# Optimization experiments

Hardware: AMD Instinct MI355X
Metric: run time of the kernel (lower is better)

Reference implementation:

```python
import jax, jax.numpy as jnp
import numpy as np

HIDDEN = 2048
NUM_HEADS = 16
HEAD_DIM = HIDDEN // NUM_HEADS


def setup_inputs() -> dict:
    key = jax.random.key(0)
    ks = jax.random.split(key, 10)
    B, S = 2, 2048
    scale = 1.0 / np.sqrt(HIDDEN)
    inp = {
        "x": jax.random.normal(ks[0], (B, S, HIDDEN), dtype=jnp.float32),
        "attention_mask": jnp.zeros((B, S), dtype=jnp.float32),
        "Wq": jax.random.normal(ks[1], (HIDDEN, HIDDEN), dtype=jnp.float32) * scale,
        "bq": jnp.zeros((HIDDEN,), dtype=jnp.float32),
        "Wk": jax.random.normal(ks[2], (HIDDEN, HIDDEN), dtype=jnp.float32) * scale,
        "bk": jnp.zeros((HIDDEN,), dtype=jnp.float32),
        "Wv": jax.random.normal(ks[3], (HIDDEN, HIDDEN), dtype=jnp.float32) * scale,
        "bv": jnp.zeros((HIDDEN,), dtype=jnp.float32),
        "Wo": jax.random.normal(ks[4], (HIDDEN, HIDDEN), dtype=jnp.float32) * scale,
        "bo": jnp.zeros((HIDDEN,), dtype=jnp.float32),
    }
    return inp


def _split_heads(t):
    # [B, S, H*D] -> [B, H, S, D]
    B, S, _ = t.shape
    return t.reshape(B, S, NUM_HEADS, HEAD_DIM).transpose(0, 2, 1, 3)


def reference(x, attention_mask, Wq, bq, Wk, bk, Wv, bv, Wo, bo):
    B, S, _ = x.shape
    # Linear layers: y = x @ W^T + b (torch nn.Linear convention)
    q = _split_heads(x @ Wq.T + bq)  # [B, H, S, D]
    k = _split_heads(x @ Wk.T + bk)
    v = _split_heads(x @ Wv.T + bv)
    scale = 1.0 / jnp.sqrt(jnp.asarray(HEAD_DIM, dtype=x.dtype))
    scores = jnp.einsum("bhqd,bhkd->bhqk", q, k) * scale  # [B, H, S, S]
    scores = scores + attention_mask[:, None, None, :]  # additive mask broadcast
    attn = jax.nn.softmax(scores, axis=-1)
    out = jnp.einsum("bhqk,bhkd->bhqd", attn, v)  # [B, H, S, D]
    out = out.transpose(0, 2, 1, 3).reshape(B, S, HIDDEN)
    return out @ Wo.T + bo
```

## Files before the change

kernel.cpp:

```cpp
#include <hip/hip_runtime.h>
#include <math.h>

constexpr int S_LEN = 2048;
constexpr int HID   = 2048;
constexpr int NH    = 16;
constexpr int HD    = 128;

typedef __attribute__((ext_vector_type(8))) short short8;
typedef __attribute__((ext_vector_type(4))) float floatx4;

static __device__ __forceinline__ ushort f2bf(float f) {
  union { float f; unsigned u; } v; v.f = f;
  unsigned r = (v.u + 0x7fffu + ((v.u >> 16) & 1u)) >> 16;
  return (ushort)r;
}
static __device__ __forceinline__ ushort f2bf_fast(float f) {
  union { float f; unsigned u; } v; v.f = f;
  return (ushort)((v.u + 0x8000u) >> 16);
}

static __device__ __forceinline__ void glds16(const ushort* g, ushort* l) {
  __builtin_amdgcn_global_load_lds(
      (const __attribute__((address_space(1))) void*)g,
      (__attribute__((address_space(3))) void*)l, 16, 0, 0);
}

static __device__ __forceinline__ void barrier_raw() {
  __builtin_amdgcn_s_barrier();
  asm volatile("" ::: "memory");
}

static __device__ __forceinline__ void cvt4(ushort* dst, const float* src, size_t i) {
  const float4 v = ((const float4*)src)[i];
  ushort4 u = {f2bf(v.x), f2bf(v.y), f2bf(v.z), f2bf(v.w)};
  ((ushort4*)dst)[i] = u;
}

__global__ __launch_bounds__(256)
void convert_all(const float* __restrict__ x,
                 const float* __restrict__ wq, const float* __restrict__ wk,
                 const float* __restrict__ wv, const float* __restrict__ wo,
                 ushort* __restrict__ xb, ushort* __restrict__ wqb,
                 ushort* __restrict__ wkb, ushort* __restrict__ wvb,
                 ushort* __restrict__ wob) {
  const size_t gid = blockIdx.x * 256 + threadIdx.x;
  const size_t T = gridDim.x * 256;
  const size_t NX = (size_t)4096 * HID / 4;
  const size_t NW = (size_t)HID * HID / 4;
  for (size_t i = gid; i < NX; i += T) cvt4(xb, x, i);
  for (size_t i = gid; i < NW; i += T) {
    cvt4(wqb, wq, i);
    cvt4(wkb, wk, i);
    cvt4(wvb, wv, i);
    cvt4(wob, wo, i);
  }
}

template <int MODE>
__device__ __forceinline__
void gemm8_core(ushort* __restrict__ lds,
                const ushort* __restrict__ A, const ushort* __restrict__ W,
                const float* __restrict__ bias, void* __restrict__ Cv,
                int m0, int n0) {
  constexpr int NT = HID / 64;

  const int tid  = threadIdx.x;
  const int lane = tid & 63;
  const int w    = tid >> 6;
  const int wm   = w >> 1, wn = w & 1;
  const int n16  = lane & 15, q4 = lane >> 4;
  const int n7   = n16 & 7;

  const int srow  = lane >> 3;
  const int sslot = lane & 7;
  const int sl    = sslot ^ srow;

  const ushort* asrc[4];
  const ushort* bsrc[2];
  #pragma unroll
  for (int c = 0; c < 4; ++c)
    asrc[c] = A + (size_t)(m0 + c*64 + w*8 + srow) * HID + sl*8;
  #pragma unroll
  for (int c = 0; c < 2; ++c)
    bsrc[c] = W + (size_t)(n0 + c*64 + w*8 + srow) * HID + sl*8;

  const int wofs = w * 512;

  floatx4 acc[4][4];
  #pragma unroll
  for (int i = 0; i < 4; ++i)
    #pragma unroll
    for (int j = 0; j < 4; ++j) acc[i][j] = (floatx4)0.f;

  auto stage_tile = [&](int t, ushort* base) {
    #pragma unroll
    for (int c = 0; c < 4; ++c)
      glds16(asrc[c] + (size_t)t*64, base + c*4096 + wofs);
    #pragma unroll
    for (int c = 0; c < 2; ++c)
      glds16(bsrc[c] + (size_t)t*64, base + 16384 + c*4096 + wofs);
  };

  stage_tile(0, lds);
  stage_tile(1, lds + 24576);

  for (int t = 0; t < NT; ++t) {
    if (t == NT - 1) asm volatile("s_waitcnt vmcnt(0)" ::: "memory");
    else             asm volatile("s_waitcnt vmcnt(6)" ::: "memory");
    barrier_raw();

    if (t + 2 < NT) stage_tile(t + 2, lds + (size_t)((t + 2) % 3) * 24576);

    const ushort* cA = lds + (size_t)(t % 3) * 24576;
    const ushort* cB = cA + 16384;

    short8 af[2][4], bf[2][4];
    #pragma unroll
    for (int kc = 0; kc < 2; ++kc) {
      #pragma unroll
      for (int mt = 0; mt < 4; ++mt)
        af[kc][mt] = *(const short8*)(cA + (wm*64 + mt*16 + n16)*64
                                         + (((kc*4 + q4) ^ n7) * 8));
      #pragma unroll
      for (int nt = 0; nt < 4; ++nt)
        bf[kc][nt] = *(const short8*)(cB + (wn*64 + nt*16 + n16)*64
                                         + (((kc*4 + q4) ^ n7) * 8));
    }
    #pragma unroll
    for (int kc = 0; kc < 2; ++kc) {
      __builtin_amdgcn_s_setprio(1);
      #pragma unroll
      for (int mt = 0; mt < 4; ++mt)
        #pragma unroll
        for (int nt = 0; nt < 4; ++nt)
          acc[mt][nt] = __builtin_amdgcn_mfma_f32_16x16x32_bf16(
              af[kc][mt], bf[kc][nt], acc[mt][nt], 0, 0, 0);
      __builtin_amdgcn_s_setprio(0);
    }
  }

  float bv4[4];
  #pragma unroll
  for (int nt = 0; nt < 4; ++nt) bv4[nt] = bias[n0 + wn*64 + nt*16 + n16];

  if constexpr (MODE == 2) {
    barrier_raw();
    ushort* dumpT = lds;
    constexpr int SP = 264;
    #pragma unroll
    for (int mt = 0; mt < 4; ++mt)
      #pragma unroll
      for (int nt = 0; nt < 4; ++nt) {
        uint2 pk;
        pk.x = (uint)f2bf(acc[mt][nt][0] + bv4[nt]) |
               ((uint)f2bf(acc[mt][nt][1] + bv4[nt]) << 16);
        pk.y = (uint)f2bf(acc[mt][nt][2] + bv4[nt]) |
               ((uint)f2bf(acc[mt][nt][3] + bv4[nt]) << 16);
        const int dl  = wn*64 + nt*16 + n16;
        const int sl0 = wm*64 + mt*16 + q4*4;
        *(uint2*)&dumpT[dl*SP + sl0] = pk;
      }
    barrier_raw();
    const int dl = (w & 1)*64 + lane;
    const int s0 = (w >> 1)*64;
    ushort* dp = (ushort*)Cv +
        ((size_t)((m0 >> 11)*NH + (n0 >> 7))*HD + dl)*S_LEN + (m0 & 2047) + s0;
    #pragma unroll
    for (int j = 0; j < 8; ++j)
      *(uint4*)&dp[j*8] = *(const uint4*)&dumpT[dl*SP + s0 + j*8];
  } else {
    #pragma unroll
    for (int mt = 0; mt < 4; ++mt)
      #pragma unroll
      for (int nt = 0; nt < 4; ++nt)
        #pragma unroll
        for (int r = 0; r < 4; ++r) {
          const int row = m0 + wm*64 + mt*16 + q4*4 + r;
          const int col = n0 + wn*64 + nt*16 + n16;
          if (MODE == 1)
            ((ushort*)Cv)[(size_t)row * HID + col] = f2bf(acc[mt][nt][r] + bv4[nt]);
          else
            ((float*)Cv)[(size_t)row * HID + col] = acc[mt][nt][r] + bv4[nt];
        }
  }
}

static __device__ __forceinline__ void tile_coords(int& m0, int& n0) {
  const int id = blockIdx.y * gridDim.x + blockIdx.x;
  const int s  = ((id & 7) << 5) | (id >> 3);
  m0 = (s >> 4) * 256;
  n0 = (s & 15) * 128;
}

__global__ __launch_bounds__(512, 2)
void gemm_qkv(const ushort* __restrict__ xb,
              const ushort* __restrict__ wqb, const ushort* __restrict__ wkb,
              const ushort* __restrict__ wvb,
              const float* __restrict__ bq, const float* __restrict__ bk,
              const float* __restrict__ bv,
              ushort* __restrict__ qb, ushort* __restrict__ kb_,
              ushort* __restrict__ vt) {
  __shared__ __align__(16) ushort lds[73728];
  int m0, n0; tile_coords(m0, n0);
  if (blockIdx.z == 0)      gemm8_core<1>(lds, xb, wqb, bq, qb,  m0, n0);
  else if (blockIdx.z == 1) gemm8_core<1>(lds, xb, wkb, bk, kb_, m0, n0);
  else                      gemm8_core<2>(lds, xb, wvb, bv, vt,  m0, n0);
}

__global__ __launch_bounds__(512, 2)
void gemm_o(const ushort* __restrict__ ao, const ushort* __restrict__ wob,
            const float* __restrict__ bo, float* __restrict__ out) {
  __shared__ __align__(16) ushort lds[73728];
  int m0, n0; tile_coords(m0, n0);
  gemm8_core<0>(lds, ao, wob, bo, out, m0, n0);
}

__global__ __launch_bounds__(256, 2)
void attn_mfma(const ushort* __restrict__ qb, const ushort* __restrict__ kbuf,
               const ushort* __restrict__ vtb, const float* __restrict__ mask,
               ushort* __restrict__ ao) {
  __shared__ __align__(16) ushort SM[25600];

  const int tid  = threadIdx.x;
  const int w    = tid >> 6;
  const int lane = tid & 63;
  const int n16  = lane & 15;
  const int q4   = lane >> 4;
  const int n7   = n16 & 7;
  const int b  = blockIdx.y >> 4;
  const int h  = blockIdx.y & 15;
  const int q0 = blockIdx.x * 128;
  const float scale = 0.08838834764831845f;

  ushort* Ks = SM;
  ushort* Vs = SM + 8192;
  ushort* Pw = SM + 16384 + w * 2304;

  short8 aq[2][4];
  #pragma unroll
  for (int mt = 0; mt < 2; ++mt) {
    const ushort* qrow = qb + (size_t)(b*S_LEN + q0 + w*32 + mt*16 + n16)*HID + h*HD;
    #pragma unroll
    for (int kc = 0; kc < 4; ++kc)
      aq[mt][kc] = *(const short8*)(qrow + kc*32 + q4*8);
  }

  const ushort* ksrc[4];
  const ushort* vsrc[4];
  #pragma unroll
  for (int i = 0; i < 4; ++i) {
    const int p = (w*4 + i)*64 + lane;
    { const int rho = p >> 4, pc = p & 15;
      const int cl = (pc & 8) | ((pc ^ rho) & 7);
      ksrc[i] = kbuf + (size_t)(b*S_LEN + rho)*HID + h*HD + cl*8; }
    { const int rho = p >> 3, pc = p & 7;
      const int cl = (pc ^ rho) & 7;
      vsrc[i] = vtb + ((size_t)(b*NH + h)*HD + rho)*S_LEN + cl*8; }
  }

  floatx4 oacc[2][8];
  float lp[2][4];
  #pragma unroll
  for (int mt = 0; mt < 2; ++mt) {
    #pragma unroll
    for (int dt = 0; dt < 8; ++dt) oacc[mt][dt] = (floatx4)0.f;
    #pragma unroll
    for (int r = 0; r < 4; ++r) lp[mt][r] = 0.f;
  }

  #pragma unroll
  for (int i = 0; i < 4; ++i) glds16(ksrc[i], Ks + (w*4 + i)*512);
  #pragma unroll
  for (int i = 0; i < 4; ++i) glds16(vsrc[i], Vs + (w*4 + i)*512);

  for (int kb0 = 0; kb0 < S_LEN; kb0 += 64) {
    const int knext = (kb0 + 64 < S_LEN) ? kb0 + 64 : kb0;

    asm volatile("s_waitcnt vmcnt(4)" ::: "memory");
    barrier_raw();

    float mk[4];
    #pragma unroll
    for (int nt = 0; nt < 4; ++nt)
      mk[nt] = mask[(size_t)b*S_LEN + kb0 + nt*16 + n16];

    floatx4 acc[2][4];
    #pragma unroll
    for (int mt = 0; mt < 2; ++mt)
      #pragma unroll
      for (int nt = 0; nt < 4; ++nt) acc[mt][nt] = (floatx4)0.f;
    __builtin_amdgcn_s_setprio(1);
    #pragma unroll
    for (int nt = 0; nt < 4; ++nt) {
      #pragma unroll
      for (int kc = 0; kc < 4; ++kc) {
        const int cl = kc*4 + q4;
        const int pc = (cl & 8) | ((cl ^ n7) & 7);
        const short8 bk = *(const short8*)&Ks[(nt*16 + n16)*128 + pc*8];
        acc[0][nt] = __builtin_amdgcn_mfma_f32_16x16x32_bf16(aq[0][kc], bk, acc[0][nt], 0, 0, 0);
        acc[1][nt] = __builtin_amdgcn_mfma_f32_16x16x32_bf16(aq[1][kc], bk, acc[1][nt], 0, 0, 0);
      }
    }
    __builtin_amdgcn_s_setprio(0);

    barrier_raw();
    #pragma unroll
    for (int i = 0; i < 4; ++i)
      glds16(ksrc[i] + (size_t)knext * HID, Ks + (w*4 + i)*512);

    #pragma unroll
    for (int mt = 0; mt < 2; ++mt)
      #pragma unroll
      for (int r = 0; r < 4; ++r) {
        float p[4];
        #pragma unroll
        for (int nt = 0; nt < 4; ++nt) p[nt] = __expf(acc[mt][nt][r] * scale + mk[nt]);
        lp[mt][r] += (p[0] + p[1]) + (p[2] + p[3]);
        #pragma unroll
        for (int nt = 0; nt < 4; ++nt)
          Pw[(mt*16 + q4*4 + r)*72 + nt*16 + n16] = f2bf_fast(p[nt]);
      }

    asm volatile("s_waitcnt vmcnt(4)" ::: "memory");
    barrier_raw();

    __builtin_amdgcn_s_setprio(1);
    #pragma unroll
    for (int kc2 = 0; kc2 < 2; ++kc2) {
      const short8 ap0 = *(const short8*)&Pw[(0*16 + n16)*72 + kc2*32 + q4*8];
      const short8 ap1 = *(const short8*)&Pw[(1*16 + n16)*72 + kc2*32 + q4*8];
      const int clb = kc2*4 + q4;
      const int pcb = (clb ^ n7) & 7;
      #pragma unroll
      for (int dt = 0; dt < 8; ++dt) {
        const short8 bvf = *(const short8*)&Vs[(dt*16 + n16)*64 + pcb*8];
        oacc[0][dt] = __builtin_amdgcn_mfma_f32_16x16x32_bf16(ap0, bvf, oacc[0][dt], 0, 0, 0);
        oacc[1][dt] = __builtin_amdgcn_mfma_f32_16x16x32_bf16(ap1, bvf, oacc[1][dt], 0, 0, 0);
      }
    }
    __builtin_amdgcn_s_setprio(0);

    barrier_raw();
    #pragma unroll
    for (int i = 0; i < 4; ++i)
      glds16(vsrc[i] + knext, Vs + (w*4 + i)*512);
  }

  #pragma unroll
  for (int mt = 0; mt < 2; ++mt)
    #pragma unroll
    for (int r = 0; r < 4; ++r) {
      float l = lp[mt][r];
      l += __shfl_xor(l, 1);
      l += __shfl_xor(l, 2);
      l += __shfl_xor(l, 4);
      l += __shfl_xor(l, 8);
      lp[mt][r] = 1.0f / l;
    }

  __syncthreads();
  ushort* dump = SM + w * 4352;
  #pragma unroll
  for (int mt = 0; mt < 2; ++mt)
    #pragma unroll
    for (int r = 0; r < 4; ++r) {
      const int row = mt*16 + q4*4 + r;
      #pragma unroll
      for (int dt = 0; dt < 8; ++dt)
        dump[row*136 + dt*16 + n16] = f2bf(oacc[mt][dt][r] * lp[mt][r]);
    }
  const int drow = lane >> 1, dhalf = lane & 1;
  const size_t gbase = (size_t)(b*S_LEN + q0 + w*32 + drow)*HID + h*HD + dhalf*64;
  #pragma unroll
  for (int j = 0; j < 8; ++j)
    *(uint4*)&ao[gbase + j*8] = *(const uint4*)&dump[drow*136 + dhalf*64 + j*8];
}

extern "C" void kernel_launch(void* const* d_in, const int* in_sizes, int n_in,
                              void* d_out, int out_size, void* d_ws, size_t ws_size,
                              hipStream_t stream) {
  (void)n_in; (void)out_size; (void)ws_size;
  const float* x    = (const float*)d_in[0];
  const float* mask = (const float*)d_in[1];
  const float* Wq   = (const float*)d_in[2];
  const float* bq   = (const float*)d_in[3];
  const float* Wk   = (const float*)d_in[4];
  const float* bk   = (const float*)d_in[5];
  const float* Wv   = (const float*)d_in[6];
  const float* bv   = (const float*)d_in[7];
  const float* Wo   = (const float*)d_in[8];
  const float* bo   = (const float*)d_in[9];
  float* out = (float*)d_out;

  const size_t MH = (size_t)4096 * HID;
  const size_t WW = (size_t)HID * HID;

  ushort* xb   = (ushort*)d_ws;
  ushort* wqb  = xb   + MH;
  ushort* wkb  = wqb  + WW;
  ushort* wvb  = wkb  + WW;
  ushort* wob  = wvb  + WW;
  ushort* qb   = wob  + WW;
  ushort* kbuf = qb   + MH;
  ushort* vt   = kbuf + MH;
  ushort* ao   = xb;

  convert_all<<<512, 256, 0, stream>>>(x, Wq, Wk, Wv, Wo, xb, wqb, wkb, wvb, wob);
  gemm_qkv<<<dim3(HID/128, 4096/256, 3), 512, 0, stream>>>(
      xb, wqb, wkb, wvb, bq, bk, bv, qb, kbuf, vt);
  attn_mfma<<<dim3(S_LEN/128, 2*NH), 256, 0, stream>>>(qb, kbuf, vt, mask, ao);
  gemm_o<<<dim3(HID/128, 4096/256), 512, 0, stream>>>(ao, wob, bo, out);
}
```

Baseline: 380.5 us.

## Halve GEMM K-tile to cut LDS and fold softmax scale into Q projection

The GEMM K-step drops from 64 to 32, so the triple-buffered LDS footprint is halved and launch bounds rise to 4 blocks per SM. This aims for higher occupancy to hide latency, at the cost of twice as many barriers and loop iterations with less MFMA work per sync. The 1/sqrt(d) attention scale moves into the Q projection epilogue, removing a multiply per score in the softmax. Scaling before the bf16 rounding slightly changes Q's numerics.

```diff
diff --git a/kernel.cpp b/kernel.cpp
--- a/kernel.cpp
+++ b/kernel.cpp
@@ -61,30 +61,23 @@
 void gemm8_core(ushort* __restrict__ lds,
                 const ushort* __restrict__ A, const ushort* __restrict__ W,
                 const float* __restrict__ bias, void* __restrict__ Cv,
-                int m0, int n0) {
-  constexpr int NT = HID / 64;
+                int m0, int n0, float cscale) {
+  constexpr int NT = HID / 32;
+  constexpr int BUF = 12288;
 
   const int tid  = threadIdx.x;
   const int lane = tid & 63;
   const int w    = tid >> 6;
   const int wm   = w >> 1, wn = w & 1;
   const int n16  = lane & 15, q4 = lane >> 4;
-  const int n7   = n16 & 7;
-
-  const int srow  = lane >> 3;
-  const int sslot = lane & 7;
-  const int sl    = sslot ^ srow;
-
-  const ushort* asrc[4];
-  const ushort* bsrc[2];
-  #pragma unroll
-  for (int c = 0; c < 4; ++c)
-    asrc[c] = A + (size_t)(m0 + c*64 + w*8 + srow) * HID + sl*8;
-  #pragma unroll
-  for (int c = 0; c < 2; ++c)
-    bsrc[c] = W + (size_t)(n0 + c*64 + w*8 + srow) * HID + sl*8;
-
-  const int wofs = w * 512;
+  const int n3   = n16 & 3;
+
+  const int srow = lane >> 2;
+  const int ssl  = (lane & 3) ^ (srow & 3);
+
+  const ushort* asrc0 = A + (size_t)(m0 +   0 + w*16 + srow) * HID + ssl*8;
+  const ushort* asrc1 = A + (size_t)(m0 + 128 + w*16 + srow) * HID + ssl*8;
+  const ushort* bsrc  = W + (size_t)(n0 +       w*16 + srow) * HID + ssl*8;
 
   floatx4 acc[4][4];
   #pragma unroll
@@ -93,50 +86,40 @@
     for (int j = 0; j < 4; ++j) acc[i][j] = (floatx4)0.f;
 
   auto stage_tile = [&](int t, ushort* base) {
-    #pragma unroll
-    for (int c = 0; c < 4; ++c)
-      glds16(asrc[c] + (size_t)t*64, base + c*4096 + wofs);
-    #pragma unroll
-    for (int c = 0; c < 2; ++c)
-      glds16(bsrc[c] + (size_t)t*64, base + 16384 + c*4096 + wofs);
+    glds16(asrc0 + (size_t)t*32, base + 0*4096 + w*512);
+    glds16(asrc1 + (size_t)t*32, base + 1*4096 + w*512);
+    glds16(bsrc  + (size_t)t*32, base + 8192  + w*512);
   };
 
   stage_tile(0, lds);
-  stage_tile(1, lds + 24576);
+  stage_tile(1, lds + BUF);
 
   for (int t = 0; t < NT; ++t) {
     if (t == NT - 1) asm volatile("s_waitcnt vmcnt(0)" ::: "memory");
-    else             asm volatile("s_waitcnt vmcnt(6)" ::: "memory");
-    barrier_raw();
-
-    if (t + 2 < NT) stage_tile(t + 2, lds + (size_t)((t + 2) % 3) * 24576);
-
-    const ushort* cA = lds + (size_t)(t % 3) * 24576;
-    const ushort* cB = cA + 16384;
-
-    short8 af[2][4], bf[2][4];
-    #pragma unroll
-    for (int kc = 0; kc < 2; ++kc) {
-      #pragma unroll
-      for (int mt = 0; mt < 4; ++mt)
-        af[kc][mt] = *(const short8*)(cA + (wm*64 + mt*16 + n16)*64
-                                         + (((kc*4 + q4) ^ n7) * 8));
+    else             asm volatile("s_waitcnt vmcnt(3)" ::: "memory");
+    barrier_raw();
+
+    if (t + 2 < NT) stage_tile(t + 2, lds + (size_t)((t + 2) % 3) * BUF);
+
+    const ushort* cA = lds + (size_t)(t % 3) * BUF;
+    const ushort* cB = cA + 8192;
+
+    short8 af[4], bf[4];
+    #pragma unroll
+    for (int mt = 0; mt < 4; ++mt)
+      af[mt] = *(const short8*)(cA + (wm*64 + mt*16 + n16)*32 + ((q4 ^ n3) * 8));
+    #pragma unroll
+    for (int nt = 0; nt < 4; ++nt)
+      bf[nt] = *(const short8*)(cB + (wn*64 + nt*16 + n16)*32 + ((q4 ^ n3) * 8));
+
+    __builtin_amdgcn_s_setprio(1);
+    #pragma unroll
+    for (int mt = 0; mt < 4; ++mt)
       #pragma unroll
       for (int nt = 0; nt < 4; ++nt)
-        bf[kc][nt] = *(const short8*)(cB + (wn*64 + nt*16 + n16)*64
-                                         + (((kc*4 + q4) ^ n7) * 8));
-    }
-    #pragma unroll
-    for (int kc = 0; kc < 2; ++kc) {
-      __builtin_amdgcn_s_setprio(1);
-      #pragma unroll
-      for (int mt = 0; mt < 4; ++mt)
-        #pragma unroll
-        for (int nt = 0; nt < 4; ++nt)
-          acc[mt][nt] = __builtin_amdgcn_mfma_f32_16x16x32_bf16(
-              af[kc][mt], bf[kc][nt], acc[mt][nt], 0, 0, 0);
-      __builtin_amdgcn_s_setprio(0);
-    }
+        acc[mt][nt] = __builtin_amdgcn_mfma_f32_16x16x32_bf16(
+            af[mt], bf[nt], acc[mt][nt], 0, 0, 0);
+    __builtin_amdgcn_s_setprio(0);
   }
 
   float bv4[4];
@@ -152,10 +135,10 @@
       #pragma unroll
       for (int nt = 0; nt < 4; ++nt) {
         uint2 pk;
-        pk.x = (uint)f2bf(acc[mt][nt][0] + bv4[nt]) |
-               ((uint)f2bf(acc[mt][nt][1] + bv4[nt]) << 16);
-        pk.y = (uint)f2bf(acc[mt][nt][2] + bv4[nt]) |
-               ((uint)f2bf(acc[mt][nt][3] + bv4[nt]) << 16);
+        pk.x = (uint)f2bf((acc[mt][nt][0] + bv4[nt]) * cscale) |
+               ((uint)f2bf((acc[mt][nt][1] + bv4[nt]) * cscale) << 16);
+        pk.y = (uint)f2bf((acc[mt][nt][2] + bv4[nt]) * cscale) |
+               ((uint)f2bf((acc[mt][nt][3] + bv4[nt]) * cscale) << 16);
         const int dl  = wn*64 + nt*16 + n16;
         const int sl0 = wm*64 + mt*16 + q4*4;
         *(uint2*)&dumpT[dl*SP + sl0] = pk;
@@ -178,7 +161,8 @@
           const int row = m0 + wm*64 + mt*16 + q4*4 + r;
           const int col = n0 + wn*64 + nt*16 + n16;
           if (MODE == 1)
-            ((ushort*)Cv)[(size_t)row * HID + col] = f2bf(acc[mt][nt][r] + bv4[nt]);
+            ((ushort*)Cv)[(size_t)row * HID + col] =
+                f2bf((acc[mt][nt][r] + bv4[nt]) * cscale);
           else
             ((float*)Cv)[(size_t)row * HID + col] = acc[mt][nt][r] + bv4[nt];
         }
@@ -192,7 +176,7 @@
   n0 = (s & 15) * 128;
 }
 
-__global__ __launch_bounds__(512, 2)
+__global__ __launch_bounds__(512, 4)
 void gemm_qkv(const ushort* __restrict__ xb,
               const ushort* __restrict__ wqb, const ushort* __restrict__ wkb,
               const ushort* __restrict__ wvb,
@@ -200,19 +184,22 @@
               const float* __restrict__ bv,
               ushort* __restrict__ qb, ushort* __restrict__ kb_,
               ushort* __restrict__ vt) {
-  __shared__ __align__(16) ushort lds[73728];
+  __shared__ __align__(16) ushort lds[36864];
   int m0, n0; tile_coords(m0, n0);
-  if (blockIdx.z == 0)      gemm8_core<1>(lds, xb, wqb, bq, qb,  m0, n0);
-  else if (blockIdx.z == 1) gemm8_core<1>(lds, xb, wkb, bk, kb_, m0, n0);
-  else                      gemm8_core<2>(lds, xb, wvb, bv, vt,  m0, n0);
-}
-
-__global__ __launch_bounds__(512, 2)
+  if (blockIdx.z == 0)
+    gemm8_core<1>(lds, xb, wqb, bq, qb,  m0, n0, 0.08838834764831845f);
+  else if (blockIdx.z == 1)
+    gemm8_core<1>(lds, xb, wkb, bk, kb_, m0, n0, 1.0f);
+  else
+    gemm8_core<2>(lds, xb, wvb, bv, vt,  m0, n0, 1.0f);
+}
+
+__global__ __launch_bounds__(512, 4)
 void gemm_o(const ushort* __restrict__ ao, const ushort* __restrict__ wob,
             const float* __restrict__ bo, float* __restrict__ out) {
-  __shared__ __align__(16) ushort lds[73728];
+  __shared__ __align__(16) ushort lds[36864];
   int m0, n0; tile_coords(m0, n0);
-  gemm8_core<0>(lds, ao, wob, bo, out, m0, n0);
+  gemm8_core<0>(lds, ao, wob, bo, out, m0, n0, 1.0f);
 }
 
 __global__ __launch_bounds__(256, 2)
@@ -230,7 +217,6 @@
   const int b  = blockIdx.y >> 4;
   const int h  = blockIdx.y & 15;
   const int q0 = blockIdx.x * 128;
-  const float scale = 0.08838834764831845f;
 
   ushort* Ks = SM;
   ushort* Vs = SM + 8192;
@@ -314,7 +300,7 @@
       for (int r = 0; r < 4; ++r) {
         float p[4];
         #pragma unroll
-        for (int nt = 0; nt < 4; ++nt) p[nt] = __expf(acc[mt][nt][r] * scale + mk[nt]);
+        for (int nt = 0; nt < 4; ++nt) p[nt] = __expf(acc[mt][nt][r] + mk[nt]);
         lp[mt][r] += (p[0] + p[1]) + (p[2] + p[3]);
         #pragma unroll
         for (int nt = 0; nt < 4; ++nt)
```

Measured after the change: 392.8 us. 3.2% more time.
